# Performance work log

Measured on AMD Instinct MI355X. Metric: run time of the kernel, lower is better.

The kernel has to match this reference:

```python
import jax, jax.numpy as jnp
import numpy as np

B, S, D, H = 16, 2048, 128, 4
HD = D // H  # 32
EPS = 1e-5


def layer_norm(x, g, b):
    m = jnp.mean(x, axis=-1, keepdims=True)
    v = jnp.mean((x - m) ** 2, axis=-1, keepdims=True)
    return (x - m) * jax.lax.rsqrt(v + EPS) * g + b


def setup_inputs() -> dict:
    key = jax.random.key(0)
    ks = jax.random.split(key, 9)
    lin = lambda k: jax.random.normal(k, (D, D), dtype=jnp.float32) * 0.01  # [in, out]
    return {
        "input0": jax.random.normal(ks[0], (B, S, D), dtype=jnp.float32),
        "Wq": lin(ks[1]), "bq": jnp.zeros((D,), jnp.float32),
        "Wk": lin(ks[2]), "bk": jnp.zeros((D,), jnp.float32),
        "Wv": lin(ks[3]), "bv": jnp.zeros((D,), jnp.float32),
        "Wo": lin(ks[4]), "bo": jnp.zeros((D,), jnp.float32),
        "g1": jnp.ones((D,), jnp.float32), "b1": jnp.zeros((D,), jnp.float32),
        "W1": lin(ks[5]), "bf1": jnp.zeros((D,), jnp.float32),
        "W2": lin(ks[6]), "bf2": jnp.zeros((D,), jnp.float32),
        "g2": jnp.ones((D,), jnp.float32), "b2": jnp.zeros((D,), jnp.float32),
    }


def reference(input0, Wq, bq, Wk, bk, Wv, bv, Wo, bo, g1, b1, W1, bf1, W2, bf2, g2, b2):
    x = input0
    # multi-head attention (self-attention), dropout in eval mode (identity)
    q = (x @ Wq + bq).reshape(B, S, H, HD)
    k = (x @ Wk + bk).reshape(B, S, H, HD)
    v = (x @ Wv + bv).reshape(B, S, H, HD)
    scores = jnp.einsum("bqhd,bkhd->bhqk", q, k) / jnp.sqrt(jnp.float32(HD))
    weights = jax.nn.softmax(scores, axis=-1)
    attn = jnp.einsum("bhqk,bkhd->bqhd", weights, v).reshape(B, S, D)
    attn = attn @ Wo + bo
    attended = layer_norm(attn + x, g1, b1)
    # feed-forward; note residual uses x (not attended), faithful to source
    ff = jax.nn.relu(attended @ W1 + bf1) @ W2 + bf2
    return layer_norm(ff + x, g2, b2)
```

## Files before the change

kernel.cpp:

```cpp
#include <hip/hip_runtime.h>
#include <math.h>

#define NB   16
#define NS   2048
#define ND   128
#define NH   4
#define NHD  32
#define NROWS (NB * NS)

typedef unsigned short u16;
typedef __bf16 bf16x8 __attribute__((ext_vector_type(8)));
typedef float  f32x4  __attribute__((ext_vector_type(4)));
typedef float  f32x16 __attribute__((ext_vector_type(16)));

static __device__ __forceinline__ u16 f2bf(float a) {
    union { __bf16 h; u16 u; } t; t.h = (__bf16)a; return t.u;
}
static __device__ __forceinline__ unsigned int pk2(float a, float b) {
    union { __bf16 h[2]; unsigned int u; } t;
    t.h[0] = (__bf16)a; t.h[1] = (__bf16)b; return t.u;
}

#if __has_builtin(__builtin_amdgcn_exp2f)
#define EXP2(x) __builtin_amdgcn_exp2f(x)
#else
extern "C" __device__ float __ocml_native_exp2_f32(float);
#define EXP2(x) __ocml_native_exp2_f32(x)
#endif

#define QSCALE (0.17677669529663687f * 1.4426950408889634f)

__global__ __launch_bounds__(256) void prep_kernel(
    const float* __restrict__ Wq, const float* __restrict__ Wk,
    const float* __restrict__ Wv, const float* __restrict__ Wo,
    const float* __restrict__ W1, const float* __restrict__ W2,
    u16* __restrict__ wt)
{
    const int wb = blockIdx.x, tid = threadIdx.x;
    const int widx = wb >> 3, sub = wb & 7;
    const float* W = widx == 0 ? Wq : widx == 1 ? Wk : widx == 2 ? Wv
                   : widx == 3 ? Wo : widx == 4 ? W1 : W2;
    const int flat8 = sub * 256 + tid;
    const int n = flat8 >> 4, k0 = (flat8 & 15) * 8;
    float v[8];
    #pragma unroll
    for (int j = 0; j < 8; ++j) v[j] = W[(size_t)(k0 + j) * ND + n];
    int4 o;
    o.x = pk2(v[0], v[1]); o.y = pk2(v[2], v[3]);
    o.z = pk2(v[4], v[5]); o.w = pk2(v[6], v[7]);
    *reinterpret_cast<int4*>(wt + (size_t)widx * 16384 + (size_t)n * ND + k0) = o;
}

__global__ __launch_bounds__(256) void qkv_mfma_kernel(
    const float* __restrict__ x,
    const u16* __restrict__ wtq, const u16* __restrict__ wtk, const u16* __restrict__ wtv,
    const float* __restrict__ bq, const float* __restrict__ bk, const float* __restrict__ bv,
    u16* __restrict__ qdm, u16* __restrict__ kfo, u16* __restrict__ vfo)
{
    __shared__ __align__(16) u16 tileK[64][136];

    const int tid = threadIdx.x, lane = tid & 63, w = tid >> 6;
    const int n = lane & 15, c = lane >> 4;
    const int row0 = blockIdx.x * 64;
    const int grow = row0 + w * 16;

    bf16x8 a[4];
    #pragma unroll
    for (int kk = 0; kk < 4; ++kk) {
        const float* xp = x + (size_t)(grow + n) * ND + kk * 32 + c * 8;
        float4 f0 = *reinterpret_cast<const float4*>(xp);
        float4 f1 = *reinterpret_cast<const float4*>(xp + 4);
        union { unsigned int u[4]; bf16x8 v; } t;
        t.u[0] = pk2(f0.x, f0.y); t.u[1] = pk2(f0.z, f0.w);
        t.u[2] = pk2(f1.x, f1.y); t.u[3] = pk2(f1.z, f1.w);
        a[kk] = t.v;
    }

    f32x4 accq[8], acck[8], accv[8];
    #pragma unroll
    for (int nb = 0; nb < 8; ++nb) {
        accq[nb] = f32x4{0.f, 0.f, 0.f, 0.f};
        acck[nb] = f32x4{0.f, 0.f, 0.f, 0.f};
        accv[nb] = f32x4{0.f, 0.f, 0.f, 0.f};
    }

    #pragma unroll
    for (int kk = 0; kk < 4; ++kk) {
        #pragma unroll
        for (int nb = 0; nb < 8; ++nb) {
            const size_t boff = (size_t)(nb * 16 + n) * ND + kk * 32 + c * 8;
            bf16x8 bqf = *reinterpret_cast<const bf16x8*>(wtq + boff);
            bf16x8 bkf = *reinterpret_cast<const bf16x8*>(wtk + boff);
            bf16x8 bvf = *reinterpret_cast<const bf16x8*>(wtv + boff);
            accq[nb] = __builtin_amdgcn_mfma_f32_16x16x32_bf16(a[kk], bqf, accq[nb], 0, 0, 0);
            acck[nb] = __builtin_amdgcn_mfma_f32_16x16x32_bf16(a[kk], bkf, acck[nb], 0, 0, 0);
            accv[nb] = __builtin_amdgcn_mfma_f32_16x16x32_bf16(a[kk], bvf, accv[nb], 0, 0, 0);
        }
    }

    const int b    = row0 >> 11;
    const int sp0b = row0 & (NS - 1);
    const int sp0  = sp0b + w * 16;

    #pragma unroll
    for (int nb = 0; nb < 8; ++nb) {
        const int col = nb * 16 + n, hh = col >> 5, d32 = col & 31;
        const float bqv = bq[col], bkv = bk[col], bvv = bv[col];
        const size_t kvb = ((size_t)b * NH + hh) * (NS * NHD);

        float q0 = (accq[nb][0] + bqv) * QSCALE;
        float q1 = (accq[nb][1] + bqv) * QSCALE;
        float q2 = (accq[nb][2] + bqv) * QSCALE;
        float q3 = (accq[nb][3] + bqv) * QSCALE;
        *reinterpret_cast<uint2*>(qdm + kvb + (size_t)d32 * NS + sp0 + 4 * c) =
            make_uint2(pk2(q0, q1), pk2(q2, q3));

        #pragma unroll
        for (int r = 0; r < 4; ++r)
            tileK[w * 16 + 4 * c + r][col] = f2bf(acck[nb][r] + bkv);

        const int lanep = d32 + 32 * (c & 1);
        const int j0    = 4 * (c >> 1);
        float v0 = accv[nb][0] + bvv, v1 = accv[nb][1] + bvv;
        float v2 = accv[nb][2] + bvv, v3 = accv[nb][3] + bvv;
        *reinterpret_cast<uint2*>(
            vfo + kvb + (size_t)(sp0 >> 4) * 512 + (size_t)lanep * 8 + j0) =
            make_uint2(pk2(v0, v1), pk2(v2, v3));
    }

    __syncthreads();

    {
        const int lk = w * 16 + (lane >> 2);
        const int gk = sp0b + lk;
        const int T = gk >> 5, l5 = gk & 31;
        #pragma unroll
        for (int i = 0; i < 4; ++i) {
            const int m16  = (lane & 3) + 4 * i;
            const int col0 = m16 * 8;
            const int hh = col0 >> 5, d32 = col0 & 31;
            const int s = d32 >> 4, c2 = (d32 >> 3) & 1;
            const size_t kvb = ((size_t)b * NH + hh) * (NS * NHD);
            int4 vv = *reinterpret_cast<const int4*>(&tileK[lk][col0]);
            *reinterpret_cast<int4*>(
                kfo + kvb + (size_t)(T * 2 + s) * 512 + (size_t)(l5 + 32 * c2) * 8) = vv;
        }
    }
}

__global__ __launch_bounds__(256) void attn_mfma_kernel(
    const u16* __restrict__ qdm,
    const u16* __restrict__ kfg,
    const u16* __restrict__ vfg,
    u16* __restrict__ ao)
{
    __shared__ float Ol[2][64][17];
    __shared__ float Dl[2][64];

    const int tid = threadIdx.x, lane = tid & 63, w = tid >> 6;
    const int qhalf = w >> 1, khalf = w & 1;

    const int bid  = blockIdx.x;
    const int bh   = (bid & 7) * 8 + ((bid >> 3) & 7);
    const int qblk = bid >> 6;
    const int b = bh >> 2, h = bh & 3;
    const int n = lane & 31, hf = lane >> 5;
    const size_t fbase = (size_t)bh * (NS * NHD);
    const int q0w = qblk * 64 + qhalf * 32;

    union { u16 h[8]; bf16x8 v; } q0u, q1u;
    {
        const u16* qb = qdm + fbase + (q0w + n);
        #pragma unroll
        for (int i = 0; i < 8; ++i) {
            q0u.h[i] = qb[(size_t)(8 * hf + i) * NS];
            q1u.h[i] = qb[(size_t)(16 + 8 * hf + i) * NS];
        }
    }
    const bf16x8 qf0 = q0u.v, qf1 = q1u.v;

    f32x16 ot, zz;
    #pragma unroll
    for (int i = 0; i < 16; ++i) { ot[i] = 0.f; zz[i] = 0.f; }
    float lp0 = 0.f, lp1 = 0.f;

    const u16* kf = kfg + fbase + (size_t)lane * 8 + (size_t)khalf * 32768;
    const u16* vf = vfg + fbase + (size_t)lane * 8 + (size_t)khalf * 32768;

    bf16x8 ka0 = *reinterpret_cast<const bf16x8*>(kf);
    bf16x8 ka1 = *reinterpret_cast<const bf16x8*>(kf + 512);
    bf16x8 va0 = *reinterpret_cast<const bf16x8*>(vf);
    bf16x8 va1 = *reinterpret_cast<const bf16x8*>(vf + 512);

    for (int t = 0; t < 32; ++t) {
        kf += 1024; vf += 1024;

        __builtin_amdgcn_s_setprio(1);
        f32x16 s = __builtin_amdgcn_mfma_f32_32x32x16_bf16(ka0, qf0, zz, 0, 0, 0);
        s = __builtin_amdgcn_mfma_f32_32x32x16_bf16(ka1, qf1, s, 0, 0, 0);
        __builtin_amdgcn_s_setprio(0);

        bf16x8 nka0 = *reinterpret_cast<const bf16x8*>(kf);
        bf16x8 nka1 = *reinterpret_cast<const bf16x8*>(kf + 512);

        union { unsigned int u[4]; bf16x8 v; } pw0, pw1;
        #pragma unroll
        for (int i = 0; i < 8; ++i) {
            float p0 = EXP2(s[2 * i]);
            float p1 = EXP2(s[2 * i + 1]);
            lp0 += p0; lp1 += p1;
            if (i < 4) pw0.u[i] = pk2(p0, p1);
            else       pw1.u[i - 4] = pk2(p0, p1);
        }

        __builtin_amdgcn_s_setprio(1);
        ot = __builtin_amdgcn_mfma_f32_32x32x16_bf16(va0, pw0.v, ot, 0, 0, 0);
        ot = __builtin_amdgcn_mfma_f32_32x32x16_bf16(va1, pw1.v, ot, 0, 0, 0);
        __builtin_amdgcn_s_setprio(0);

        va0 = *reinterpret_cast<const bf16x8*>(vf);
        va1 = *reinterpret_cast<const bf16x8*>(vf + 512);
        ka0 = nka0; ka1 = nka1;
    }

    float lp  = lp0 + lp1;
    float lpt = lp + __shfl_xor(lp, 32);

    if (khalf) {
        #pragma unroll
        for (int i = 0; i < 16; ++i) Ol[qhalf][lane][i] = ot[i];
        Dl[qhalf][lane] = lpt;
    }
    __syncthreads();
    if (!khalf) {
        #pragma unroll
        for (int i = 0; i < 16; ++i) ot[i] += Ol[qhalf][lane][i];
        const float dn  = lpt + Dl[qhalf][lane];
        const float inv = 1.0f / dn;

        u16* orow = ao + ((size_t)b * NS + q0w + n) * ND + h * NHD + 4 * hf;
        #pragma unroll
        for (int g = 0; g < 4; ++g) {
            uint2 wv = make_uint2(pk2(ot[4 * g] * inv, ot[4 * g + 1] * inv),
                                  pk2(ot[4 * g + 2] * inv, ot[4 * g + 3] * inv));
            *reinterpret_cast<uint2*>(orow + 8 * g) = wv;
        }
    }
}

__global__ __launch_bounds__(256) void tail_kernel(
    const u16* __restrict__ A0, const u16* __restrict__ wto,
    const u16* __restrict__ wt1, const u16* __restrict__ wt2,
    const float* __restrict__ bo, const float* __restrict__ bf1,
    const float* __restrict__ bf2, const float* __restrict__ x,
    const float* __restrict__ g1, const float* __restrict__ b1,
    const float* __restrict__ g2, const float* __restrict__ b2,
    float* __restrict__ outp)
{
    __shared__ __align__(16) u16 tile[64][136];
    const int tid = threadIdx.x, lane = tid & 63, w = tid >> 6;
    const int n = lane & 15, c = lane >> 4;
    const int row0 = blockIdx.x * 64;
    const int grow = row0 + w * 16;
    const int lrow = w * 16;

    bf16x8 a[4];
    f32x4 acc[8];

    #pragma unroll
    for (int kk = 0; kk < 4; ++kk)
        a[kk] = *reinterpret_cast<const bf16x8*>(
            A0 + (size_t)(grow + n) * ND + kk * 32 + c * 8);
    #pragma unroll
    for (int nb = 0; nb < 8; ++nb) acc[nb] = f32x4{0.f, 0.f, 0.f, 0.f};
    #pragma unroll
    for (int kk = 0; kk < 4; ++kk)
        #pragma unroll
        for (int nb = 0; nb < 8; ++nb) {
            bf16x8 bw = *reinterpret_cast<const bf16x8*>(
                wto + (size_t)(nb * 16 + n) * ND + kk * 32 + c * 8);
            acc[nb] = __builtin_amdgcn_mfma_f32_16x16x32_bf16(a[kk], bw, acc[nb], 0, 0, 0);
        }

    {
        float vals[8][4];
        float sr[4]  = {0.f, 0.f, 0.f, 0.f};
        float sr2[4] = {0.f, 0.f, 0.f, 0.f};
        #pragma unroll
        for (int nb = 0; nb < 8; ++nb) {
            const int col = nb * 16 + n;
            const float bb = bo[col];
            #pragma unroll
            for (int r = 0; r < 4; ++r) {
                float vv = acc[nb][r] + bb +
                           x[(size_t)(grow + 4 * c + r) * ND + col];
                vals[nb][r] = vv;
                sr[r]  += vv;
                sr2[r] += vv * vv;
            }
        }
        #pragma unroll
        for (int m = 1; m < 16; m <<= 1)
            #pragma unroll
            for (int r = 0; r < 4; ++r) {
                sr[r]  += __shfl_xor(sr[r],  m);
                sr2[r] += __shfl_xor(sr2[r], m);
            }
        #pragma unroll
        for (int r = 0; r < 4; ++r) {
            float mean = sr[r] * (1.f / 128.f);
            float var  = fmaf(-mean, mean, sr2[r] * (1.f / 128.f));
            float rstd = rsqrtf(var + 1e-5f);
            #pragma unroll
            for (int nb = 0; nb < 8; ++nb) {
                const int col = nb * 16 + n;
                float y = fmaf((vals[nb][r] - mean) * rstd, g1[col], b1[col]);
                tile[lrow + 4 * c + r][col] = f2bf(y);
            }
        }
    }
    __syncthreads();

    #pragma unroll
    for (int kk = 0; kk < 4; ++kk)
        a[kk] = *reinterpret_cast<const bf16x8*>(&tile[lrow + n][kk * 32 + c * 8]);
    __syncthreads();
    #pragma unroll
    for (int nb = 0; nb < 8; ++nb) acc[nb] = f32x4{0.f, 0.f, 0.f, 0.f};
    #pragma unroll
    for (int kk = 0; kk < 4; ++kk)
        #pragma unroll
        for (int nb = 0; nb < 8; ++nb) {
            bf16x8 bw = *reinterpret_cast<const bf16x8*>(
                wt1 + (size_t)(nb * 16 + n) * ND + kk * 32 + c * 8);
            acc[nb] = __builtin_amdgcn_mfma_f32_16x16x32_bf16(a[kk], bw, acc[nb], 0, 0, 0);
        }
    #pragma unroll
    for (int nb = 0; nb < 8; ++nb) {
        const int col = nb * 16 + n;
        const float bb = bf1[col];
        #pragma unroll
        for (int r = 0; r < 4; ++r)
            tile[lrow + 4 * c + r][col] = f2bf(fmaxf(acc[nb][r] + bb, 0.f));
    }
    __syncthreads();

    #pragma unroll
    for (int kk = 0; kk < 4; ++kk)
        a[kk] = *reinterpret_cast<const bf16x8*>(&tile[lrow + n][kk * 32 + c * 8]);
    #pragma unroll
    for (int nb = 0; nb < 8; ++nb) acc[nb] = f32x4{0.f, 0.f, 0.f, 0.f};
    #pragma unroll
    for (int kk = 0; kk < 4; ++kk)
        #pragma unroll
        for (int nb = 0; nb < 8; ++nb) {
            bf16x8 bw = *reinterpret_cast<const bf16x8*>(
                wt2 + (size_t)(nb * 16 + n) * ND + kk * 32 + c * 8);
            acc[nb] = __builtin_amdgcn_mfma_f32_16x16x32_bf16(a[kk], bw, acc[nb], 0, 0, 0);
        }
    {
        float vals[8][4];
        float sr[4]  = {0.f, 0.f, 0.f, 0.f};
        float sr2[4] = {0.f, 0.f, 0.f, 0.f};
        #pragma unroll
        for (int nb = 0; nb < 8; ++nb) {
            const int col = nb * 16 + n;
            const float bb = bf2[col];
            #pragma unroll
            for (int r = 0; r < 4; ++r) {
                float vv = acc[nb][r] + bb +
                           x[(size_t)(grow + 4 * c + r) * ND + col];
                vals[nb][r] = vv;
                sr[r]  += vv;
                sr2[r] += vv * vv;
            }
        }
        #pragma unroll
        for (int m = 1; m < 16; m <<= 1)
            #pragma unroll
            for (int r = 0; r < 4; ++r) {
                sr[r]  += __shfl_xor(sr[r],  m);
                sr2[r] += __shfl_xor(sr2[r], m);
            }
        #pragma unroll
        for (int r = 0; r < 4; ++r) {
            float mean = sr[r] * (1.f / 128.f);
            float var  = fmaf(-mean, mean, sr2[r] * (1.f / 128.f));
            float rstd = rsqrtf(var + 1e-5f);
            #pragma unroll
            for (int nb = 0; nb < 8; ++nb) {
                const int col = nb * 16 + n;
                float y = fmaf((vals[nb][r] - mean) * rstd, g2[col], b2[col]);
                outp[(size_t)(grow + 4 * c + r) * ND + col] = y;
            }
        }
    }
}

extern "C" void kernel_launch(void* const* d_in, const int* in_sizes, int n_in,
                              void* d_out, int out_size, void* d_ws, size_t ws_size,
                              hipStream_t stream)
{
    const float* x   = (const float*)d_in[0];
    const float* Wq  = (const float*)d_in[1];
    const float* bq  = (const float*)d_in[2];
    const float* Wk  = (const float*)d_in[3];
    const float* bk  = (const float*)d_in[4];
    const float* Wv  = (const float*)d_in[5];
    const float* bv  = (const float*)d_in[6];
    const float* Wo  = (const float*)d_in[7];
    const float* bo  = (const float*)d_in[8];
    const float* g1  = (const float*)d_in[9];
    const float* b1  = (const float*)d_in[10];
    const float* W1  = (const float*)d_in[11];
    const float* bf1 = (const float*)d_in[12];
    const float* W2  = (const float*)d_in[13];
    const float* bf2 = (const float*)d_in[14];
    const float* g2  = (const float*)d_in[15];
    const float* b2  = (const float*)d_in[16];
    float* outp = (float*)d_out;

    const size_t NE = (size_t)NROWS * ND;
    u16* wt  = (u16*)d_ws;
    u16* qb  = wt + 6 * 16384;
    u16* kfb = qb + NE;
    u16* vfb = kfb + NE;
    u16* aob = vfb + NE;

    dim3 blk(256);
    prep_kernel<<<dim3(48), blk, 0, stream>>>(Wq, Wk, Wv, Wo, W1, W2, wt);
    qkv_mfma_kernel<<<dim3(NROWS / 64), blk, 0, stream>>>(
        x, wt + 0 * 16384, wt + 1 * 16384, wt + 2 * 16384, bq, bk, bv, qb, kfb, vfb);
    attn_mfma_kernel<<<dim3(2048), blk, 0, stream>>>(qb, kfb, vfb, aob);
    tail_kernel<<<dim3(NROWS / 64), blk, 0, stream>>>(
        aob, wt + 3 * 16384, wt + 4 * 16384, wt + 5 * 16384,
        bo, bf1, bf2, x, g1, b1, g2, b2, outp);
}
```

Baseline: 125.2 us.

## Software-pipeline attention QK/PV MFMAs and store Q row-major via LDS

The attention inner loop is restructured into a two-stage software pipeline. The QK^T MFMAs for the next key tile are issued together with the PV MFMAs for the current tile, so the exp2/pack work can overlap with matrix-core work, with a prologue and epilogue around the loop. Separately, Q is now staged through shared memory in the QKV kernel and written row-major per head, which lets the attention kernel load Q fragments as 16-byte vector loads instead of 16 strided scalar loads. The cost is more live registers for the double-buffered K/V/P fragments and a second LDS tile in the QKV kernel. The block barrier before the tile read-back is also dropped, since each wave only reads rows it wrote itself.

```diff
diff --git a/kernel.cpp b/kernel.cpp
--- a/kernel.cpp
+++ b/kernel.cpp
@@ -55,8 +55,9 @@
     const float* __restrict__ x,
     const u16* __restrict__ wtq, const u16* __restrict__ wtk, const u16* __restrict__ wtv,
     const float* __restrict__ bq, const float* __restrict__ bk, const float* __restrict__ bv,
-    u16* __restrict__ qdm, u16* __restrict__ kfo, u16* __restrict__ vfo)
+    u16* __restrict__ qo, u16* __restrict__ kfo, u16* __restrict__ vfo)
 {
+    __shared__ __align__(16) u16 tileQ[64][136];
     __shared__ __align__(16) u16 tileK[64][136];
 
     const int tid = threadIdx.x, lane = tid & 63, w = tid >> 6;
@@ -108,16 +109,11 @@
         const float bqv = bq[col], bkv = bk[col], bvv = bv[col];
         const size_t kvb = ((size_t)b * NH + hh) * (NS * NHD);
 
-        float q0 = (accq[nb][0] + bqv) * QSCALE;
-        float q1 = (accq[nb][1] + bqv) * QSCALE;
-        float q2 = (accq[nb][2] + bqv) * QSCALE;
-        float q3 = (accq[nb][3] + bqv) * QSCALE;
-        *reinterpret_cast<uint2*>(qdm + kvb + (size_t)d32 * NS + sp0 + 4 * c) =
-            make_uint2(pk2(q0, q1), pk2(q2, q3));
-
-        #pragma unroll
-        for (int r = 0; r < 4; ++r)
+        #pragma unroll
+        for (int r = 0; r < 4; ++r) {
+            tileQ[w * 16 + 4 * c + r][col] = f2bf((accq[nb][r] + bqv) * QSCALE);
             tileK[w * 16 + 4 * c + r][col] = f2bf(acck[nb][r] + bkv);
+        }
 
         const int lanep = d32 + 32 * (c & 1);
         const int j0    = 4 * (c >> 1);
@@ -128,8 +124,6 @@
             make_uint2(pk2(v0, v1), pk2(v2, v3));
     }
 
-    __syncthreads();
-
     {
         const int lk = w * 16 + (lane >> 2);
         const int gk = sp0b + lk;
@@ -141,15 +135,17 @@
             const int hh = col0 >> 5, d32 = col0 & 31;
             const int s = d32 >> 4, c2 = (d32 >> 3) & 1;
             const size_t kvb = ((size_t)b * NH + hh) * (NS * NHD);
-            int4 vv = *reinterpret_cast<const int4*>(&tileK[lk][col0]);
+            int4 qv = *reinterpret_cast<const int4*>(&tileQ[lk][col0]);
+            *reinterpret_cast<int4*>(qo + kvb + (size_t)gk * NHD + d32) = qv;
+            int4 kv = *reinterpret_cast<const int4*>(&tileK[lk][col0]);
             *reinterpret_cast<int4*>(
-                kfo + kvb + (size_t)(T * 2 + s) * 512 + (size_t)(l5 + 32 * c2) * 8) = vv;
+                kfo + kvb + (size_t)(T * 2 + s) * 512 + (size_t)(l5 + 32 * c2) * 8) = kv;
         }
     }
 }
 
 __global__ __launch_bounds__(256) void attn_mfma_kernel(
-    const u16* __restrict__ qdm,
+    const u16* __restrict__ qg,
     const u16* __restrict__ kfg,
     const u16* __restrict__ vfg,
     u16* __restrict__ ao)
@@ -168,16 +164,10 @@
     const size_t fbase = (size_t)bh * (NS * NHD);
     const int q0w = qblk * 64 + qhalf * 32;
 
-    union { u16 h[8]; bf16x8 v; } q0u, q1u;
-    {
-        const u16* qb = qdm + fbase + (q0w + n);
-        #pragma unroll
-        for (int i = 0; i < 8; ++i) {
-            q0u.h[i] = qb[(size_t)(8 * hf + i) * NS];
-            q1u.h[i] = qb[(size_t)(16 + 8 * hf + i) * NS];
-        }
-    }
-    const bf16x8 qf0 = q0u.v, qf1 = q1u.v;
+    const bf16x8 qf0 = *reinterpret_cast<const bf16x8*>(
+        qg + fbase + (size_t)(q0w + n) * NHD + 8 * hf);
+    const bf16x8 qf1 = *reinterpret_cast<const bf16x8*>(
+        qg + fbase + (size_t)(q0w + n) * NHD + 16 + 8 * hf);
 
     f32x16 ot, zz;
     #pragma unroll
@@ -187,40 +177,76 @@
     const u16* kf = kfg + fbase + (size_t)lane * 8 + (size_t)khalf * 32768;
     const u16* vf = vfg + fbase + (size_t)lane * 8 + (size_t)khalf * 32768;
 
-    bf16x8 ka0 = *reinterpret_cast<const bf16x8*>(kf);
-    bf16x8 ka1 = *reinterpret_cast<const bf16x8*>(kf + 512);
-    bf16x8 va0 = *reinterpret_cast<const bf16x8*>(vf);
-    bf16x8 va1 = *reinterpret_cast<const bf16x8*>(vf + 512);
-
-    for (int t = 0; t < 32; ++t) {
-        kf += 1024; vf += 1024;
-
+    auto LDK = [&](int t, int half) {
+        return *reinterpret_cast<const bf16x8*>(kf + (size_t)t * 1024 + half * 512);
+    };
+    auto LDV = [&](int t, int half) {
+        return *reinterpret_cast<const bf16x8*>(vf + (size_t)t * 1024 + half * 512);
+    };
+    auto EXPPACK = [&](const f32x16& s, bf16x8& w0, bf16x8& w1) {
+        union { unsigned int u[4]; bf16x8 v; } a0, a1;
+        #pragma unroll
+        for (int i = 0; i < 4; ++i) {
+            float p0 = EXP2(s[2 * i]), p1 = EXP2(s[2 * i + 1]);
+            lp0 += p0; lp1 += p1;
+            a0.u[i] = pk2(p0, p1);
+        }
+        #pragma unroll
+        for (int i = 4; i < 8; ++i) {
+            float p0 = EXP2(s[2 * i]), p1 = EXP2(s[2 * i + 1]);
+            lp0 += p0; lp1 += p1;
+            a1.u[i - 4] = pk2(p0, p1);
+        }
+        w0 = a0.v; w1 = a1.v;
+    };
+
+    bf16x8 kA0 = LDK(0, 0), kA1 = LDK(0, 1);
+    bf16x8 vA0 = LDV(0, 0), vA1 = LDV(0, 1);
+    f32x16 s;
+    s = __builtin_amdgcn_mfma_f32_32x32x16_bf16(kA0, qf0, zz, 0, 0, 0);
+    s = __builtin_amdgcn_mfma_f32_32x32x16_bf16(kA1, qf1, s, 0, 0, 0);
+    bf16x8 kB0 = LDK(1, 0), kB1 = LDK(1, 1);
+    bf16x8 pA0, pA1;
+    EXPPACK(s, pA0, pA1);
+
+    for (int j = 0; j < 15; ++j) {
+        const int t = 2 * j;
+        bf16x8 vB0 = LDV(t + 1, 0), vB1 = LDV(t + 1, 1);
+        bf16x8 nk0 = LDK(t + 2, 0), nk1 = LDK(t + 2, 1);
         __builtin_amdgcn_s_setprio(1);
-        f32x16 s = __builtin_amdgcn_mfma_f32_32x32x16_bf16(ka0, qf0, zz, 0, 0, 0);
-        s = __builtin_amdgcn_mfma_f32_32x32x16_bf16(ka1, qf1, s, 0, 0, 0);
+        s  = __builtin_amdgcn_mfma_f32_32x32x16_bf16(kB0, qf0, zz, 0, 0, 0);
+        s  = __builtin_amdgcn_mfma_f32_32x32x16_bf16(kB1, qf1, s, 0, 0, 0);
+        ot = __builtin_amdgcn_mfma_f32_32x32x16_bf16(vA0, pA0, ot, 0, 0, 0);
+        ot = __builtin_amdgcn_mfma_f32_32x32x16_bf16(vA1, pA1, ot, 0, 0, 0);
         __builtin_amdgcn_s_setprio(0);
-
-        bf16x8 nka0 = *reinterpret_cast<const bf16x8*>(kf);
-        bf16x8 nka1 = *reinterpret_cast<const bf16x8*>(kf + 512);
-
-        union { unsigned int u[4]; bf16x8 v; } pw0, pw1;
-        #pragma unroll
-        for (int i = 0; i < 8; ++i) {
-            float p0 = EXP2(s[2 * i]);
-            float p1 = EXP2(s[2 * i + 1]);
-            lp0 += p0; lp1 += p1;
-            if (i < 4) pw0.u[i] = pk2(p0, p1);
-            else       pw1.u[i - 4] = pk2(p0, p1);
-        }
-
+        bf16x8 pB0, pB1;
+        EXPPACK(s, pB0, pB1);
+
+        vA0 = LDV(t + 2, 0); vA1 = LDV(t + 2, 1);
+        kB0 = LDK(t + 3, 0); kB1 = LDK(t + 3, 1);
         __builtin_amdgcn_s_setprio(1);
-        ot = __builtin_amdgcn_mfma_f32_32x32x16_bf16(va0, pw0.v, ot, 0, 0, 0);
-        ot = __builtin_amdgcn_mfma_f32_32x32x16_bf16(va1, pw1.v, ot, 0, 0, 0);
+        s  = __builtin_amdgcn_mfma_f32_32x32x16_bf16(nk0, qf0, zz, 0, 0, 0);
+        s  = __builtin_amdgcn_mfma_f32_32x32x16_bf16(nk1, qf1, s, 0, 0, 0);
+        ot = __builtin_amdgcn_mfma_f32_32x32x16_bf16(vB0, pB0, ot, 0, 0, 0);
+        ot = __builtin_amdgcn_mfma_f32_32x32x16_bf16(vB1, pB1, ot, 0, 0, 0);
         __builtin_amdgcn_s_setprio(0);
-
-        va0 = *reinterpret_cast<const bf16x8*>(vf);
-        va1 = *reinterpret_cast<const bf16x8*>(vf + 512);
-        ka0 = nka0; ka1 = nka1;
+        EXPPACK(s, pA0, pA1);
+    }
+
+    {
+        bf16x8 vB0 = LDV(31, 0), vB1 = LDV(31, 1);
+        __builtin_amdgcn_s_setprio(1);
+        s  = __builtin_amdgcn_mfma_f32_32x32x16_bf16(kB0, qf0, zz, 0, 0, 0);
+        s  = __builtin_amdgcn_mfma_f32_32x32x16_bf16(kB1, qf1, s, 0, 0, 0);
+        ot = __builtin_amdgcn_mfma_f32_32x32x16_bf16(vA0, pA0, ot, 0, 0, 0);
+        ot = __builtin_amdgcn_mfma_f32_32x32x16_bf16(vA1, pA1, ot, 0, 0, 0);
+        __builtin_amdgcn_s_setprio(0);
+        bf16x8 pB0, pB1;
+        EXPPACK(s, pB0, pB1);
+        __builtin_amdgcn_s_setprio(1);
+        ot = __builtin_amdgcn_mfma_f32_32x32x16_bf16(vB0, pB0, ot, 0, 0, 0);
+        ot = __builtin_amdgcn_mfma_f32_32x32x16_bf16(vB1, pB1, ot, 0, 0, 0);
+        __builtin_amdgcn_s_setprio(0);
     }
 
     float lp  = lp0 + lp1;
```

Result: no change. 125.9 us (+0.6%).

## Split attention KV across four waves, row-major Q, and MFMA denominators

Applied to the files above, without the earlier changes.

The QKV kernel now stages Q through shared memory and writes it row-major per head, dropping the block barrier because each wave reads back only its own rows. Attention blocks now cover 32 queries, with the four waves each taking a quarter of the keys, and the grid doubles. This gives contiguous vector Q loads and more blocks in flight. The softmax denominator is computed with extra MFMAs against a ones matrix instead of VALU sums, and the tail kernel preloads the x residual once and reuses it for both layer norms. The trade-offs are more MFMA work per step, a three-way LDS reduction at the end, and higher register pressure in the tail.

```diff
diff --git a/kernel.cpp b/kernel.cpp
--- a/kernel.cpp
+++ b/kernel.cpp
@@ -55,8 +55,9 @@
     const float* __restrict__ x,
     const u16* __restrict__ wtq, const u16* __restrict__ wtk, const u16* __restrict__ wtv,
     const float* __restrict__ bq, const float* __restrict__ bk, const float* __restrict__ bv,
-    u16* __restrict__ qdm, u16* __restrict__ kfo, u16* __restrict__ vfo)
+    u16* __restrict__ qo, u16* __restrict__ kfo, u16* __restrict__ vfo)
 {
+    __shared__ __align__(16) u16 tileQ[64][136];
     __shared__ __align__(16) u16 tileK[64][136];
 
     const int tid = threadIdx.x, lane = tid & 63, w = tid >> 6;
@@ -108,16 +109,11 @@
         const float bqv = bq[col], bkv = bk[col], bvv = bv[col];
         const size_t kvb = ((size_t)b * NH + hh) * (NS * NHD);
 
-        float q0 = (accq[nb][0] + bqv) * QSCALE;
-        float q1 = (accq[nb][1] + bqv) * QSCALE;
-        float q2 = (accq[nb][2] + bqv) * QSCALE;
-        float q3 = (accq[nb][3] + bqv) * QSCALE;
-        *reinterpret_cast<uint2*>(qdm + kvb + (size_t)d32 * NS + sp0 + 4 * c) =
-            make_uint2(pk2(q0, q1), pk2(q2, q3));
-
-        #pragma unroll
-        for (int r = 0; r < 4; ++r)
+        #pragma unroll
+        for (int r = 0; r < 4; ++r) {
+            tileQ[w * 16 + 4 * c + r][col] = f2bf((accq[nb][r] + bqv) * QSCALE);
             tileK[w * 16 + 4 * c + r][col] = f2bf(acck[nb][r] + bkv);
+        }
 
         const int lanep = d32 + 32 * (c & 1);
         const int j0    = 4 * (c >> 1);
@@ -128,8 +124,6 @@
             make_uint2(pk2(v0, v1), pk2(v2, v3));
     }
 
-    __syncthreads();
-
     {
         const int lk = w * 16 + (lane >> 2);
         const int gk = sp0b + lk;
@@ -141,24 +135,25 @@
             const int hh = col0 >> 5, d32 = col0 & 31;
             const int s = d32 >> 4, c2 = (d32 >> 3) & 1;
             const size_t kvb = ((size_t)b * NH + hh) * (NS * NHD);
-            int4 vv = *reinterpret_cast<const int4*>(&tileK[lk][col0]);
+            int4 qv = *reinterpret_cast<const int4*>(&tileQ[lk][col0]);
+            *reinterpret_cast<int4*>(qo + kvb + (size_t)gk * NHD + d32) = qv;
+            int4 kv = *reinterpret_cast<const int4*>(&tileK[lk][col0]);
             *reinterpret_cast<int4*>(
-                kfo + kvb + (size_t)(T * 2 + s) * 512 + (size_t)(l5 + 32 * c2) * 8) = vv;
+                kfo + kvb + (size_t)(T * 2 + s) * 512 + (size_t)(l5 + 32 * c2) * 8) = kv;
         }
     }
 }
 
 __global__ __launch_bounds__(256) void attn_mfma_kernel(
-    const u16* __restrict__ qdm,
+    const u16* __restrict__ qg,
     const u16* __restrict__ kfg,
     const u16* __restrict__ vfg,
     u16* __restrict__ ao)
 {
-    __shared__ float Ol[2][64][17];
-    __shared__ float Dl[2][64];
+    __shared__ float Ol[3][64][17];
+    __shared__ float Dl[3][64];
 
     const int tid = threadIdx.x, lane = tid & 63, w = tid >> 6;
-    const int qhalf = w >> 1, khalf = w & 1;
 
     const int bid  = blockIdx.x;
     const int bh   = (bid & 7) * 8 + ((bid >> 3) & 7);
@@ -166,33 +161,41 @@
     const int b = bh >> 2, h = bh & 3;
     const int n = lane & 31, hf = lane >> 5;
     const size_t fbase = (size_t)bh * (NS * NHD);
-    const int q0w = qblk * 64 + qhalf * 32;
-
-    union { u16 h[8]; bf16x8 v; } q0u, q1u;
-    {
-        const u16* qb = qdm + fbase + (q0w + n);
-        #pragma unroll
-        for (int i = 0; i < 8; ++i) {
-            q0u.h[i] = qb[(size_t)(8 * hf + i) * NS];
-            q1u.h[i] = qb[(size_t)(16 + 8 * hf + i) * NS];
-        }
-    }
-    const bf16x8 qf0 = q0u.v, qf1 = q1u.v;
-
-    f32x16 ot, zz;
-    #pragma unroll
-    for (int i = 0; i < 16; ++i) { ot[i] = 0.f; zz[i] = 0.f; }
-    float lp0 = 0.f, lp1 = 0.f;
-
-    const u16* kf = kfg + fbase + (size_t)lane * 8 + (size_t)khalf * 32768;
-    const u16* vf = vfg + fbase + (size_t)lane * 8 + (size_t)khalf * 32768;
+    const int q0w = qblk * 32;
+
+    const bf16x8 qf0 = *reinterpret_cast<const bf16x8*>(
+        qg + fbase + (size_t)(q0w + n) * NHD + 8 * hf);
+    const bf16x8 qf1 = *reinterpret_cast<const bf16x8*>(
+        qg + fbase + (size_t)(q0w + n) * NHD + 16 + 8 * hf);
+
+    union { unsigned int u[4]; bf16x8 v; } ONES;
+    ONES.u[0] = 0x3F803F80u; ONES.u[1] = 0x3F803F80u;
+    ONES.u[2] = 0x3F803F80u; ONES.u[3] = 0x3F803F80u;
+
+    f32x16 ot, dn, zz;
+    #pragma unroll
+    for (int i = 0; i < 16; ++i) { ot[i] = 0.f; dn[i] = 0.f; zz[i] = 0.f; }
+
+    const u16* kf = kfg + fbase + (size_t)lane * 8 + (size_t)w * 16384;
+    const u16* vf = vfg + fbase + (size_t)lane * 8 + (size_t)w * 16384;
+
+    auto EXPPACK = [&](const f32x16& s, bf16x8& w0, bf16x8& w1) {
+        union { unsigned int u[4]; bf16x8 v; } a0, a1;
+        #pragma unroll
+        for (int i = 0; i < 4; ++i)
+            a0.u[i] = pk2(EXP2(s[2 * i]), EXP2(s[2 * i + 1]));
+        #pragma unroll
+        for (int i = 0; i < 4; ++i)
+            a1.u[i] = pk2(EXP2(s[8 + 2 * i]), EXP2(s[9 + 2 * i]));
+        w0 = a0.v; w1 = a1.v;
+    };
 
     bf16x8 ka0 = *reinterpret_cast<const bf16x8*>(kf);
     bf16x8 ka1 = *reinterpret_cast<const bf16x8*>(kf + 512);
     bf16x8 va0 = *reinterpret_cast<const bf16x8*>(vf);
     bf16x8 va1 = *reinterpret_cast<const bf16x8*>(vf + 512);
 
-    for (int t = 0; t < 32; ++t) {
+    for (int t = 0; t < 16; ++t) {
         kf += 1024; vf += 1024;
 
         __builtin_amdgcn_s_setprio(1);
@@ -203,19 +206,14 @@
         bf16x8 nka0 = *reinterpret_cast<const bf16x8*>(kf);
         bf16x8 nka1 = *reinterpret_cast<const bf16x8*>(kf + 512);
 
-        union { unsigned int u[4]; bf16x8 v; } pw0, pw1;
-        #pragma unroll
-        for (int i = 0; i < 8; ++i) {
-            float p0 = EXP2(s[2 * i]);
-            float p1 = EXP2(s[2 * i + 1]);
-            lp0 += p0; lp1 += p1;
-            if (i < 4) pw0.u[i] = pk2(p0, p1);
-            else       pw1.u[i - 4] = pk2(p0, p1);
-        }
+        bf16x8 pw0, pw1;
+        EXPPACK(s, pw0, pw1);
 
         __builtin_amdgcn_s_setprio(1);
-        ot = __builtin_amdgcn_mfma_f32_32x32x16_bf16(va0, pw0.v, ot, 0, 0, 0);
-        ot = __builtin_amdgcn_mfma_f32_32x32x16_bf16(va1, pw1.v, ot, 0, 0, 0);
+        ot = __builtin_amdgcn_mfma_f32_32x32x16_bf16(va0, pw0, ot, 0, 0, 0);
+        dn = __builtin_amdgcn_mfma_f32_32x32x16_bf16(ONES.v, pw0, dn, 0, 0, 0);
+        ot = __builtin_amdgcn_mfma_f32_32x32x16_bf16(va1, pw1, ot, 0, 0, 0);
+        dn = __builtin_amdgcn_mfma_f32_32x32x16_bf16(ONES.v, pw1, dn, 0, 0, 0);
         __builtin_amdgcn_s_setprio(0);
 
         va0 = *reinterpret_cast<const bf16x8*>(vf);
@@ -223,20 +221,19 @@
         ka0 = nka0; ka1 = nka1;
     }
 
-    float lp  = lp0 + lp1;
-    float lpt = lp + __shfl_xor(lp, 32);
-
-    if (khalf) {
-        #pragma unroll
-        for (int i = 0; i < 16; ++i) Ol[qhalf][lane][i] = ot[i];
-        Dl[qhalf][lane] = lpt;
+    if (w > 0) {
+        #pragma unroll
+        for (int i = 0; i < 16; ++i) Ol[w - 1][lane][i] = ot[i];
+        Dl[w - 1][lane] = dn[0];
     }
     __syncthreads();
-    if (!khalf) {
-        #pragma unroll
-        for (int i = 0; i < 16; ++i) ot[i] += Ol[qhalf][lane][i];
-        const float dn  = lpt + Dl[qhalf][lane];
-        const float inv = 1.0f / dn;
+    if (w == 0) {
+        #pragma unroll
+        for (int j = 0; j < 3; ++j)
+            #pragma unroll
+            for (int i = 0; i < 16; ++i) ot[i] += Ol[j][lane][i];
+        const float dnt = dn[0] + Dl[0][lane] + Dl[1][lane] + Dl[2][lane];
+        const float inv = 1.0f / dnt;
 
         u16* orow = ao + ((size_t)b * NS + q0w + n) * ND + h * NHD + 4 * hf;
         #pragma unroll
@@ -267,6 +264,15 @@
     bf16x8 a[4];
     f32x4 acc[8];
 
+    float xres[8][4];
+    #pragma unroll
+    for (int nb = 0; nb < 8; ++nb) {
+        const int col = nb * 16 + n;
+        #pragma unroll
+        for (int r = 0; r < 4; ++r)
+            xres[nb][r] = x[(size_t)(grow + 4 * c + r) * ND + col];
+    }
+
     #pragma unroll
     for (int kk = 0; kk < 4; ++kk)
         a[kk] = *reinterpret_cast<const bf16x8*>(
@@ -292,8 +298,7 @@
             const float bb = bo[col];
             #pragma unroll
             for (int r = 0; r < 4; ++r) {
-                float vv = acc[nb][r] + bb +
-                           x[(size_t)(grow + 4 * c + r) * ND + col];
+                float vv = acc[nb][r] + bb + xres[nb][r];
                 vals[nb][r] = vv;
                 sr[r]  += vv;
                 sr2[r] += vv * vv;
@@ -368,8 +373,7 @@
             const float bb = bf2[col];
             #pragma unroll
             for (int r = 0; r < 4; ++r) {
-                float vv = acc[nb][r] + bb +
-                           x[(size_t)(grow + 4 * c + r) * ND + col];
+                float vv = acc[nb][r] + bb + xres[nb][r];
                 vals[nb][r] = vv;
                 sr[r]  += vv;
                 sr2[r] += vv * vv;
@@ -431,7 +435,7 @@
     prep_kernel<<<dim3(48), blk, 0, stream>>>(Wq, Wk, Wv, Wo, W1, W2, wt);
     qkv_mfma_kernel<<<dim3(NROWS / 64), blk, 0, stream>>>(
         x, wt + 0 * 16384, wt + 1 * 16384, wt + 2 * 16384, bq, bk, bv, qb, kfb, vfb);
-    attn_mfma_kernel<<<dim3(2048), blk, 0, stream>>>(qb, kfb, vfb, aob);
+    attn_mfma_kernel<<<dim3(4096), blk, 0, stream>>>(qb, kfb, vfb, aob);
     tail_kernel<<<dim3(NROWS / 64), blk, 0, stream>>>(
         aob, wt + 3 * 16384, wt + 4 * 16384, wt + 5 * 16384,
         bo, bf1, bf2, x, g1, b1, g2, b2, outp);
```

Measured after the change: 134.7 us. 1.08x slower.
